# Optimization experiments

Hardware: AMD Instinct MI355X
Metric: run time of the kernel (lower is better)

Reference implementation:

```python
import jax, jax.numpy as jnp
import numpy as np

N_NODES = 50000
N_EDGES = 800000
F_IN, HID, N_CLASS = 128, 256, 40


def setup_inputs() -> dict:
    key = jax.random.key(0)
    ks = jax.random.split(key, 8)
    scale = lambda sh: 1.0 / np.sqrt(sh[-1]).astype(np.float32)
    x = jax.random.normal(ks[0], (N_NODES, F_IN), jnp.float32)
    edge_index = jax.random.randint(ks[1], (2, N_EDGES), 0, N_NODES, dtype=jnp.int64)
    W1l = jax.random.normal(ks[2], (HID, F_IN), jnp.float32) * scale((HID, F_IN))
    W1r = jax.random.normal(ks[3], (HID, F_IN), jnp.float32) * scale((HID, F_IN))
    b1 = jax.random.normal(ks[4], (HID,), jnp.float32) * 0.01
    W2l = jax.random.normal(ks[5], (N_CLASS, HID), jnp.float32) * scale((N_CLASS, HID))
    W2r = jax.random.normal(ks[6], (N_CLASS, HID), jnp.float32) * scale((N_CLASS, HID))
    b2 = jax.random.normal(ks[7], (N_CLASS,), jnp.float32) * 0.01
    return {"x": x, "edge_index": edge_index, "W1l": W1l, "b1": b1, "W1r": W1r,
            "W2l": W2l, "b2": b2, "W2r": W2r}


def sage_conv(x, edge_index, Wl, b, Wr):
    """PyG SAGEConv: lin_l(mean_{j->i} x_j) + lin_r(x_i); bias only on lin_l."""
    src, dst = edge_index[0], edge_index[1]
    # gather source node features -> segment mean at destination
    agg = jax.ops.segment_sum(x[src], dst, num_segments=N_NODES)
    deg = jax.ops.segment_sum(jnp.ones((edge_index.shape[1],), x.dtype), dst,
                              num_segments=N_NODES)
    mean = agg / jnp.maximum(deg, 1.0)[:, None]
    return mean @ Wl.T + b + x @ Wr.T


def reference(x, edge_index, W1l, b1, W1r, W2l, b2, W2r):
    h = jax.nn.relu(sage_conv(x, edge_index, W1l, b1, W1r))
    # dropout is identity in eval mode
    logits = sage_conv(h, edge_index, W2l, b2, W2r)
    return jax.nn.log_softmax(logits, axis=1)
```

## Files before the change

kernel.cpp:

```cpp
#include <hip/hip_runtime.h>
#include <hip/hip_bf16.h>
#include <float.h>

#define NN 50000
#define NE 800000
#define FIN 128
#define HID 256
#define NC 40
#define NBKT 196
#define BCAP 5120
#define EPB 4096

typedef __attribute__((ext_vector_type(8))) short bf16x8;
typedef __attribute__((ext_vector_type(4))) float f32x4;

__device__ __forceinline__ float bf2f(unsigned short u) {
  union { unsigned int i; float f; } v; v.i = ((unsigned int)u) << 16; return v.f;
}
__device__ __forceinline__ float lo_bf(unsigned int u) {
  union { unsigned int i; float f; } v; v.i = u << 16; return v.f;
}
__device__ __forceinline__ float hi_bf(unsigned int u) {
  union { unsigned int i; float f; } v; v.i = u & 0xffff0000u; return v.f;
}
__device__ __forceinline__ unsigned short f2bf(float f) {
  union { float f; unsigned int u; } v; v.f = f;
  unsigned int u = v.u;
  unsigned int r = u + 0x7fffu + ((u >> 16) & 1u);
  return (unsigned short)(r >> 16);
}

__global__ __launch_bounds__(256) void k_prep(const float* __restrict__ x,
                                              unsigned short* __restrict__ xb,
                                              const float* __restrict__ W1l,
                                              const float* __restrict__ W1r,
                                              unsigned short* __restrict__ w1t,
                                              const float* __restrict__ W2l,
                                              const float* __restrict__ W2r,
                                              unsigned short* __restrict__ w2t) {
  int tid = blockIdx.x * 256 + threadIdx.x;
  if (tid < NN * FIN / 4) {
    float4 v = ((const float4*)x)[tid];
    ushort4 o;
    o.x = f2bf(v.x); o.y = f2bf(v.y); o.z = f2bf(v.z); o.w = f2bf(v.w);
    ((ushort4*)xb)[tid] = o;
  }
  if (tid < HID * 256) {
    int j = tid >> 8, k = tid & 255;
    float v = (k < FIN) ? W1l[j * FIN + k] : W1r[j * FIN + (k - FIN)];
    w1t[tid] = f2bf(v);
  }
  if (tid < 80 * HID) {
    int j = tid >> 8, k = tid & 255;
    float v = (j < NC) ? W2l[j * HID + k] : W2r[(j - NC) * HID + k];
    w2t[tid] = f2bf(v);
  }
}

__global__ __launch_bounds__(512) void k_part(const int* __restrict__ src,
                                              const int* __restrict__ dst,
                                              int* __restrict__ bucket_cursor,
                                              unsigned int* __restrict__ pairs) {
  __shared__ int cnt[NBKT], cbase[NBKT], cur[NBKT];
  int t = threadIdx.x;
  for (int i = t; i < NBKT; i += 512) cnt[i] = 0;
  __syncthreads();
  int base = blockIdx.x * EPB;
  int myb[8];
  unsigned int mypk[8];
  #pragma unroll
  for (int k = 0; k < 8; ++k) {
    int e = base + k * 512 + t;
    myb[k] = -1;
    if (e < NE) {
      int d = dst[e];
      int b = d >> 8;
      myb[k] = b;
      mypk[k] = (unsigned int)src[e] | ((unsigned int)(d & 255) << 24);
      atomicAdd(&cnt[b], 1);
    }
  }
  __syncthreads();
  for (int i = t; i < NBKT; i += 512) {
    cur[i] = 0;
    cbase[i] = cnt[i] ? atomicAdd(&bucket_cursor[i], cnt[i]) : 0;
  }
  __syncthreads();
  #pragma unroll
  for (int k = 0; k < 8; ++k) {
    if (myb[k] >= 0) {
      int l = atomicAdd(&cur[myb[k]], 1);
      pairs[myb[k] * BCAP + cbase[myb[k]] + l] = mypk[k];
    }
  }
}

__global__ __launch_bounds__(256) void k_bscan(const int* __restrict__ bucket_cursor,
                                               int* __restrict__ bucket_base,
                                               int* __restrict__ rowptr) {
  __shared__ int sm[256];
  int t = threadIdx.x;
  int v = (t < NBKT) ? bucket_cursor[t] : 0;
  sm[t] = v;
  __syncthreads();
  for (int off = 1; off < 256; off <<= 1) {
    int u = (t >= off) ? sm[t - off] : 0;
    __syncthreads();
    sm[t] += u;
    __syncthreads();
  }
  bucket_base[t] = sm[t] - v;
  if (t == 0) rowptr[NN] = NE;
}

__global__ __launch_bounds__(512) void k_build(const int* __restrict__ bucket_base,
                                               const unsigned int* __restrict__ pairs,
                                               int* __restrict__ rowptr,
                                               float* __restrict__ rdeg,
                                               int* __restrict__ eidx) {
  __shared__ int hist[256], lbase[256], cur[256];
  int t = threadIdx.x;
  int b = blockIdx.x;
  int bb = bucket_base[b];
  int n  = bucket_base[b + 1] - bb;
  if (t < 256) hist[t] = 0;
  __syncthreads();
  unsigned int held[10];
  #pragma unroll
  for (int k = 0; k < 10; ++k) {
    int i = t + k * 512;
    unsigned int p = 0xFFFFFFFFu;
    if (i < n) {
      p = pairs[b * BCAP + i];
      atomicAdd(&hist[p >> 24], 1);
    }
    held[k] = p;
  }
  __syncthreads();
  int v = 0;
  if (t < 256) { v = hist[t]; lbase[t] = v; }
  __syncthreads();
  for (int off = 1; off < 256; off <<= 1) {
    int u = 0;
    if (t < 256 && t >= off) u = lbase[t - off];
    __syncthreads();
    if (t < 256) lbase[t] += u;
    __syncthreads();
  }
  if (t < 256) {
    int excl = lbase[t] - v;
    cur[t] = excl;
    int node = b * 256 + t;
    if (node < NN) {
      rowptr[node] = bb + excl;
      rdeg[node] = 1.0f / fmaxf((float)v, 1.0f);
    }
  }
  __syncthreads();
  #pragma unroll
  for (int k = 0; k < 10; ++k) {
    unsigned int p = held[k];
    if (p != 0xFFFFFFFFu) {
      int l = atomicAdd(&cur[p >> 24], 1);
      eidx[bb + l] = (int)(p & 0x00FFFFFFu);
    }
  }
}

__global__ __launch_bounds__(256) void k_agg1(const int* __restrict__ rowptr,
                                              const int* __restrict__ eidx,
                                              const float* __restrict__ rdeg,
                                              const unsigned int* __restrict__ xb,
                                              unsigned int* __restrict__ mean_bf) {
  int wid = threadIdx.x >> 6, lane = threadIdx.x & 63;
  int n = blockIdx.x * 4 + wid;
  if (n >= NN) return;
  int beg = rowptr[n], end = rowptr[n + 1];
  float ax = 0.f, ay = 0.f;
  int e = beg;
  for (; e + 8 <= end; e += 8) {
    int s0 = eidx[e],     s1 = eidx[e + 1], s2 = eidx[e + 2], s3 = eidx[e + 3];
    int s4 = eidx[e + 4], s5 = eidx[e + 5], s6 = eidx[e + 6], s7 = eidx[e + 7];
    unsigned int v0 = xb[s0 * 64 + lane], v1 = xb[s1 * 64 + lane];
    unsigned int v2 = xb[s2 * 64 + lane], v3 = xb[s3 * 64 + lane];
    unsigned int v4 = xb[s4 * 64 + lane], v5 = xb[s5 * 64 + lane];
    unsigned int v6 = xb[s6 * 64 + lane], v7 = xb[s7 * 64 + lane];
    ax += ((lo_bf(v0) + lo_bf(v1)) + (lo_bf(v2) + lo_bf(v3)))
        + ((lo_bf(v4) + lo_bf(v5)) + (lo_bf(v6) + lo_bf(v7)));
    ay += ((hi_bf(v0) + hi_bf(v1)) + (hi_bf(v2) + hi_bf(v3)))
        + ((hi_bf(v4) + hi_bf(v5)) + (hi_bf(v6) + hi_bf(v7)));
  }
  for (; e < end; ++e) {
    unsigned int v = xb[eidx[e] * 64 + lane];
    ax += lo_bf(v); ay += hi_bf(v);
  }
  float r = rdeg[n];
  unsigned int o = (unsigned int)f2bf(ax * r) | ((unsigned int)f2bf(ay * r) << 16);
  mean_bf[n * 64 + lane] = o;
}

__global__ __launch_bounds__(512, 4) void k_l12(const unsigned short* __restrict__ mean_bf,
                                                const unsigned short* __restrict__ x_bf,
                                                const unsigned short* __restrict__ w1t,
                                                const float* __restrict__ b1,
                                                const unsigned short* __restrict__ w2t,
                                                const float* __restrict__ b2,
                                                unsigned short* __restrict__ yl_bf,
                                                float* __restrict__ yr) {
  __shared__ unsigned short As[64][264];
  __shared__ unsigned short Ht[64][264];
  int t = threadIdx.x;
  int lane = t & 63, wave = t >> 6;
  int i0 = blockIdx.x * 64;
  #pragma unroll
  for (int u = 0; u < 4; ++u) {
    int idx = t + u * 512;
    int row = idx >> 5, q = idx & 31, k = q * 8;
    int gi = i0 + row;
    uint4 v = make_uint4(0, 0, 0, 0);
    if (gi < NN)
      v = *(const uint4*)((k < FIN) ? (mean_bf + gi * FIN + k)
                                    : (x_bf + gi * FIN + (k - FIN)));
    *(uint4*)&As[row][q * 8] = v;
  }
  __syncthreads();
  int fr = lane & 15, fq = lane >> 4, fk = fq * 8;
  f32x4 acc[4][2] = {};
  #pragma unroll
  for (int k0 = 0; k0 < HID; k0 += 32) {
    bf16x8 a[4], b[2];
    #pragma unroll
    for (int m = 0; m < 4; ++m) a[m] = *(const bf16x8*)&As[m * 16 + fr][k0 + fk];
    #pragma unroll
    for (int n = 0; n < 2; ++n)
      b[n] = *(const bf16x8*)(w1t + (wave * 32 + n * 16 + fr) * 256 + k0 + fk);
    #pragma unroll
    for (int m = 0; m < 4; ++m)
      #pragma unroll
      for (int n = 0; n < 2; ++n)
        acc[m][n] = __builtin_amdgcn_mfma_f32_16x16x32_bf16(a[m], b[n], acc[m][n], 0, 0, 0);
  }
  #pragma unroll
  for (int n = 0; n < 2; ++n) {
    int col = wave * 32 + n * 16 + fr;
    float bias = b1[col];
    #pragma unroll
    for (int m = 0; m < 4; ++m)
      #pragma unroll
      for (int r = 0; r < 4; ++r)
        Ht[m * 16 + fq * 4 + r][col] = f2bf(fmaxf(acc[m][n][r] + bias, 0.f));
  }
  __syncthreads();
  if (wave < 5) {
    f32x4 acc2[4] = {};
    #pragma unroll
    for (int k0 = 0; k0 < HID; k0 += 32) {
      bf16x8 b = *(const bf16x8*)(w2t + (wave * 16 + fr) * 256 + k0 + fk);
      #pragma unroll
      for (int m = 0; m < 4; ++m) {
        bf16x8 a = *(const bf16x8*)&Ht[m * 16 + fr][k0 + fk];
        acc2[m] = __builtin_amdgcn_mfma_f32_16x16x32_bf16(a, b, acc2[m], 0, 0, 0);
      }
    }
    int j = wave * 16 + fr;
    float badd = (j >= NC) ? b2[j - NC] : 0.f;
    #pragma unroll
    for (int m = 0; m < 4; ++m)
      #pragma unroll
      for (int r = 0; r < 4; ++r) {
        int i = i0 + m * 16 + fq * 4 + r;
        if (i < NN) {
          if (j < NC) yl_bf[i * NC + j] = f2bf(acc2[m][r]);
          else        yr[i * NC + (j - NC)] = acc2[m][r] + badd;
        }
      }
  }
}

__global__ __launch_bounds__(256) void k_final(const int* __restrict__ rowptr,
                                               const int* __restrict__ eidx,
                                               const float* __restrict__ rdeg,
                                               const unsigned short* __restrict__ yl_bf,
                                               const float* __restrict__ yr,
                                               float* __restrict__ out) {
  int wid  = threadIdx.x >> 6;
  int lane = threadIdx.x & 63;
  int row  = blockIdx.x * 4 + wid;
  if (row >= NN) return;
  int beg = rowptr[row], end = rowptr[row + 1];
  float logit = 0.f, v = -FLT_MAX;
  if (lane < NC) {
    float acc = 0.f;
    int e = beg;
    for (; e + 8 <= end; e += 8) {
      int s0 = eidx[e],     s1 = eidx[e + 1], s2 = eidx[e + 2], s3 = eidx[e + 3];
      int s4 = eidx[e + 4], s5 = eidx[e + 5], s6 = eidx[e + 6], s7 = eidx[e + 7];
      unsigned short a0 = yl_bf[s0 * NC + lane], a1 = yl_bf[s1 * NC + lane];
      unsigned short a2 = yl_bf[s2 * NC + lane], a3 = yl_bf[s3 * NC + lane];
      unsigned short a4 = yl_bf[s4 * NC + lane], a5 = yl_bf[s5 * NC + lane];
      unsigned short a6 = yl_bf[s6 * NC + lane], a7 = yl_bf[s7 * NC + lane];
      acc += ((bf2f(a0) + bf2f(a1)) + (bf2f(a2) + bf2f(a3)))
           + ((bf2f(a4) + bf2f(a5)) + (bf2f(a6) + bf2f(a7)));
    }
    for (; e < end; ++e) acc += bf2f(yl_bf[eidx[e] * NC + lane]);
    logit = acc * rdeg[row] + yr[row * NC + lane];
    v = logit;
  }
  #pragma unroll
  for (int o = 32; o > 0; o >>= 1) v = fmaxf(v, __shfl_xor(v, o, 64));
  float m = v;
  float s = (lane < NC) ? expf(logit - m) : 0.f;
  #pragma unroll
  for (int o = 32; o > 0; o >>= 1) s += __shfl_xor(s, o, 64);
  float lse = logf(s);
  if (lane < NC) out[row * NC + lane] = logit - m - lse;
}

extern "C" void kernel_launch(void* const* d_in, const int* in_sizes, int n_in,
                              void* d_out, int out_size, void* d_ws, size_t ws_size,
                              hipStream_t stream) {
  const float* x   = (const float*)d_in[0];
  const int*   ei  = (const int*)d_in[1];
  const float* W1l = (const float*)d_in[2];
  const float* b1  = (const float*)d_in[3];
  const float* W1r = (const float*)d_in[4];
  const float* W2l = (const float*)d_in[5];
  const float* b2  = (const float*)d_in[6];
  const float* W2r = (const float*)d_in[7];
  const int* src = ei;
  const int* dst = ei + NE;

  char* ws = (char*)d_ws;
  int*            rowptr  = (int*)(ws);
  float*          rdeg    = (float*)(ws + 200064);
  int*            bcursor = (int*)(ws + 400064);
  int*            bbase   = (int*)(ws + 401088);
  unsigned int*   pairs   = (unsigned int*)(ws + 402112);
  int*            eidx    = (int*)(ws + 4416192);
  unsigned short* x_bf    = (unsigned short*)(ws + 7616192);
  unsigned short* mean_bf = (unsigned short*)(ws + 20416192);
  unsigned short* w1t     = (unsigned short*)(ws + 33216192);
  unsigned short* yl_bf   = (unsigned short*)(ws + 33347264);
  float*          yr      = (float*)(ws + 37347264);
  unsigned short* w2t     = (unsigned short*)(ws + 45347264);

  hipMemsetAsync(bcursor, 0, 1024, stream);

  k_prep<<<(NN * FIN / 4 + 255) / 256, 256, 0, stream>>>(x, x_bf, W1l, W1r, w1t,
                                                         W2l, W2r, w2t);
  k_part<<<(NE + EPB - 1) / EPB, 512, 0, stream>>>(src, dst, bcursor, pairs);
  k_bscan<<<1, 256, 0, stream>>>(bcursor, bbase, rowptr);
  k_build<<<NBKT, 512, 0, stream>>>(bbase, pairs, rowptr, rdeg, eidx);
  k_agg1<<<(NN + 3) / 4, 256, 0, stream>>>(rowptr, eidx, rdeg, (const unsigned int*)x_bf,
                                           (unsigned int*)mean_bf);
  k_l12<<<(NN + 63) / 64, 512, 0, stream>>>(mean_bf, x_bf, w1t, b1, w2t, b2, yl_bf, yr);
  k_final<<<NN / 4, 256, 0, stream>>>(rowptr, eidx, rdeg, yl_bf, yr, (float*)d_out);
}
```

Baseline: 218.3 us.

## Fuse prep with partition, fold bucket scan into build, deepen gather unroll

```diff
diff --git a/kernel.cpp b/kernel.cpp
--- a/kernel.cpp
+++ b/kernel.cpp
@@ -9,7 +9,8 @@
 #define NC 40
 #define NBKT 196
 #define BCAP 5120
-#define EPB 4096
+#define EPB 1024
+#define NPART 782
 
 typedef __attribute__((ext_vector_type(8))) short bf16x8;
 typedef __attribute__((ext_vector_type(4))) float f32x4;
@@ -30,46 +31,45 @@
   return (unsigned short)(r >> 16);
 }
 
-__global__ __launch_bounds__(256) void k_prep(const float* __restrict__ x,
-                                              unsigned short* __restrict__ xb,
-                                              const float* __restrict__ W1l,
-                                              const float* __restrict__ W1r,
-                                              unsigned short* __restrict__ w1t,
-                                              const float* __restrict__ W2l,
-                                              const float* __restrict__ W2r,
-                                              unsigned short* __restrict__ w2t) {
-  int tid = blockIdx.x * 256 + threadIdx.x;
-  if (tid < NN * FIN / 4) {
-    float4 v = ((const float4*)x)[tid];
+__global__ __launch_bounds__(512) void k_partprep(const int* __restrict__ src,
+                                                  const int* __restrict__ dst,
+                                                  int* __restrict__ bucket_cursor,
+                                                  unsigned int* __restrict__ pairs,
+                                                  const float* __restrict__ x,
+                                                  unsigned short* __restrict__ xb,
+                                                  const float* __restrict__ W1l,
+                                                  const float* __restrict__ W1r,
+                                                  unsigned short* __restrict__ w1t,
+                                                  const float* __restrict__ W2l,
+                                                  const float* __restrict__ W2r,
+                                                  unsigned short* __restrict__ w2t) {
+  const int GT = NPART * 512;
+  int gt = blockIdx.x * 512 + threadIdx.x;
+  for (int i = gt; i < NN * FIN / 4; i += GT) {
+    float4 v = ((const float4*)x)[i];
     ushort4 o;
     o.x = f2bf(v.x); o.y = f2bf(v.y); o.z = f2bf(v.z); o.w = f2bf(v.w);
-    ((ushort4*)xb)[tid] = o;
-  }
-  if (tid < HID * 256) {
-    int j = tid >> 8, k = tid & 255;
+    ((ushort4*)xb)[i] = o;
+  }
+  if (gt < HID * 256) {
+    int j = gt >> 8, k = gt & 255;
     float v = (k < FIN) ? W1l[j * FIN + k] : W1r[j * FIN + (k - FIN)];
-    w1t[tid] = f2bf(v);
-  }
-  if (tid < 80 * HID) {
-    int j = tid >> 8, k = tid & 255;
+    w1t[gt] = f2bf(v);
+  }
+  if (gt < 80 * HID) {
+    int j = gt >> 8, k = gt & 255;
     float v = (j < NC) ? W2l[j * HID + k] : W2r[(j - NC) * HID + k];
-    w2t[tid] = f2bf(v);
-  }
-}
-
-__global__ __launch_bounds__(512) void k_part(const int* __restrict__ src,
-                                              const int* __restrict__ dst,
-                                              int* __restrict__ bucket_cursor,
-                                              unsigned int* __restrict__ pairs) {
+    w2t[gt] = f2bf(v);
+  }
   __shared__ int cnt[NBKT], cbase[NBKT], cur[NBKT];
   int t = threadIdx.x;
   for (int i = t; i < NBKT; i += 512) cnt[i] = 0;
   __syncthreads();
   int base = blockIdx.x * EPB;
-  int myb[8];
-  unsigned int mypk[8];
-  #pragma unroll
-  for (int k = 0; k < 8; ++k) {
+  int myb[2];
+  unsigned int mypk[2];
+  #pragma unroll
+  for (int k = 0; k < 2; ++k) {
     int e = base + k * 512 + t;
     myb[k] = -1;
     if (e < NE) {
@@ -87,7 +87,7 @@
   }
   __syncthreads();
   #pragma unroll
-  for (int k = 0; k < 8; ++k) {
+  for (int k = 0; k < 2; ++k) {
     if (myb[k] >= 0) {
       int l = atomicAdd(&cur[myb[k]], 1);
       pairs[myb[k] * BCAP + cbase[myb[k]] + l] = mypk[k];
@@ -95,34 +95,30 @@
   }
 }
 
-__global__ __launch_bounds__(256) void k_bscan(const int* __restrict__ bucket_cursor,
-                                               int* __restrict__ bucket_base,
-                                               int* __restrict__ rowptr) {
-  __shared__ int sm[256];
-  int t = threadIdx.x;
-  int v = (t < NBKT) ? bucket_cursor[t] : 0;
-  sm[t] = v;
-  __syncthreads();
-  for (int off = 1; off < 256; off <<= 1) {
-    int u = (t >= off) ? sm[t - off] : 0;
-    __syncthreads();
-    sm[t] += u;
-    __syncthreads();
-  }
-  bucket_base[t] = sm[t] - v;
-  if (t == 0) rowptr[NN] = NE;
-}
-
-__global__ __launch_bounds__(512) void k_build(const int* __restrict__ bucket_base,
+__global__ __launch_bounds__(512) void k_build(const int* __restrict__ bucket_cursor,
                                                const unsigned int* __restrict__ pairs,
                                                int* __restrict__ rowptr,
                                                float* __restrict__ rdeg,
                                                int* __restrict__ eidx) {
+  __shared__ int sm[256];
   __shared__ int hist[256], lbase[256], cur[256];
   int t = threadIdx.x;
   int b = blockIdx.x;
-  int bb = bucket_base[b];
-  int n  = bucket_base[b + 1] - bb;
+  int c = 0;
+  if (t < 256) {
+    c = (t < NBKT) ? bucket_cursor[t] : 0;
+    sm[t] = c;
+  }
+  __syncthreads();
+  for (int off = 1; off < 256; off <<= 1) {
+    int u = 0;
+    if (t < 256 && t >= off) u = sm[t - off];
+    __syncthreads();
+    if (t < 256) sm[t] += u;
+    __syncthreads();
+  }
+  int bb = (b > 0) ? sm[b - 1] : 0;
+  int n  = sm[b] - bb;
   if (t < 256) hist[t] = 0;
   __syncthreads();
   unsigned int held[10];
@@ -156,6 +152,7 @@
       rdeg[node] = 1.0f / fmaxf((float)v, 1.0f);
     }
   }
+  if (b == NBKT - 1 && t == 0) rowptr[NN] = NE;
   __syncthreads();
   #pragma unroll
   for (int k = 0; k < 10; ++k) {
@@ -178,17 +175,29 @@
   int beg = rowptr[n], end = rowptr[n + 1];
   float ax = 0.f, ay = 0.f;
   int e = beg;
-  for (; e + 8 <= end; e += 8) {
-    int s0 = eidx[e],     s1 = eidx[e + 1], s2 = eidx[e + 2], s3 = eidx[e + 3];
-    int s4 = eidx[e + 4], s5 = eidx[e + 5], s6 = eidx[e + 6], s7 = eidx[e + 7];
-    unsigned int v0 = xb[s0 * 64 + lane], v1 = xb[s1 * 64 + lane];
-    unsigned int v2 = xb[s2 * 64 + lane], v3 = xb[s3 * 64 + lane];
-    unsigned int v4 = xb[s4 * 64 + lane], v5 = xb[s5 * 64 + lane];
-    unsigned int v6 = xb[s6 * 64 + lane], v7 = xb[s7 * 64 + lane];
-    ax += ((lo_bf(v0) + lo_bf(v1)) + (lo_bf(v2) + lo_bf(v3)))
-        + ((lo_bf(v4) + lo_bf(v5)) + (lo_bf(v6) + lo_bf(v7)));
-    ay += ((hi_bf(v0) + hi_bf(v1)) + (hi_bf(v2) + hi_bf(v3)))
-        + ((hi_bf(v4) + hi_bf(v5)) + (hi_bf(v6) + hi_bf(v7)));
+  for (; e + 16 <= end; e += 16) {
+    int s[16]; unsigned int v[16];
+    #pragma unroll
+    for (int k = 0; k < 16; ++k) s[k] = eidx[e + k];
+    #pragma unroll
+    for (int k = 0; k < 16; ++k) v[k] = xb[s[k] * 64 + lane];
+    float x0 = 0.f, x1 = 0.f, y0 = 0.f, y1 = 0.f;
+    #pragma unroll
+    for (int k = 0; k < 16; k += 2) {
+      x0 += lo_bf(v[k]);     y0 += hi_bf(v[k]);
+      x1 += lo_bf(v[k + 1]); y1 += hi_bf(v[k + 1]);
+    }
+    ax += x0 + x1; ay += y0 + y1;
+  }
+  if (e + 8 <= end) {
+    int s[8]; unsigned int v[8];
+    #pragma unroll
+    for (int k = 0; k < 8; ++k) s[k] = eidx[e + k];
+    #pragma unroll
+    for (int k = 0; k < 8; ++k) v[k] = xb[s[k] * 64 + lane];
+    #pragma unroll
+    for (int k = 0; k < 8; ++k) { ax += lo_bf(v[k]); ay += hi_bf(v[k]); }
+    e += 8;
   }
   for (; e < end; ++e) {
     unsigned int v = xb[eidx[e] * 64 + lane];
@@ -292,15 +301,26 @@
   if (lane < NC) {
     float acc = 0.f;
     int e = beg;
-    for (; e + 8 <= end; e += 8) {
-      int s0 = eidx[e],     s1 = eidx[e + 1], s2 = eidx[e + 2], s3 = eidx[e + 3];
-      int s4 = eidx[e + 4], s5 = eidx[e + 5], s6 = eidx[e + 6], s7 = eidx[e + 7];
-      unsigned short a0 = yl_bf[s0 * NC + lane], a1 = yl_bf[s1 * NC + lane];
-      unsigned short a2 = yl_bf[s2 * NC + lane], a3 = yl_bf[s3 * NC + lane];
-      unsigned short a4 = yl_bf[s4 * NC + lane], a5 = yl_bf[s5 * NC + lane];
-      unsigned short a6 = yl_bf[s6 * NC + lane], a7 = yl_bf[s7 * NC + lane];
-      acc += ((bf2f(a0) + bf2f(a1)) + (bf2f(a2) + bf2f(a3)))
-           + ((bf2f(a4) + bf2f(a5)) + (bf2f(a6) + bf2f(a7)));
+    for (; e + 16 <= end; e += 16) {
+      int s[16]; unsigned short a[16];
+      #pragma unroll
+      for (int k = 0; k < 16; ++k) s[k] = eidx[e + k];
+      #pragma unroll
+      for (int k = 0; k < 16; ++k) a[k] = yl_bf[s[k] * NC + lane];
+      float a0 = 0.f, a1 = 0.f;
+      #pragma unroll
+      for (int k = 0; k < 16; k += 2) { a0 += bf2f(a[k]); a1 += bf2f(a[k + 1]); }
+      acc += a0 + a1;
+    }
+    if (e + 8 <= end) {
+      int s[8]; unsigned short a[8];
+      #pragma unroll
+      for (int k = 0; k < 8; ++k) s[k] = eidx[e + k];
+      #pragma unroll
+      for (int k = 0; k < 8; ++k) a[k] = yl_bf[s[k] * NC + lane];
+      #pragma unroll
+      for (int k = 0; k < 8; ++k) acc += bf2f(a[k]);
+      e += 8;
     }
     for (; e < end; ++e) acc += bf2f(yl_bf[eidx[e] * NC + lane]);
     logit = acc * rdeg[row] + yr[row * NC + lane];
@@ -334,7 +354,6 @@
   int*            rowptr  = (int*)(ws);
   float*          rdeg    = (float*)(ws + 200064);
   int*            bcursor = (int*)(ws + 400064);
-  int*            bbase   = (int*)(ws + 401088);
   unsigned int*   pairs   = (unsigned int*)(ws + 402112);
   int*            eidx    = (int*)(ws + 4416192);
   unsigned short* x_bf    = (unsigned short*)(ws + 7616192);
@@ -346,11 +365,9 @@
 
   hipMemsetAsync(bcursor, 0, 1024, stream);
 
-  k_prep<<<(NN * FIN / 4 + 255) / 256, 256, 0, stream>>>(x, x_bf, W1l, W1r, w1t,
-                                                         W2l, W2r, w2t);
-  k_part<<<(NE + EPB - 1) / EPB, 512, 0, stream>>>(src, dst, bcursor, pairs);
-  k_bscan<<<1, 256, 0, stream>>>(bcursor, bbase, rowptr);
-  k_build<<<NBKT, 512, 0, stream>>>(bbase, pairs, rowptr, rdeg, eidx);
+  k_partprep<<<NPART, 512, 0, stream>>>(src, dst, bcursor, pairs,
+                                        x, x_bf, W1l, W1r, w1t, W2l, W2r, w2t);
+  k_build<<<NBKT, 512, 0, stream>>>(bcursor, pairs, rowptr, rdeg, eidx);
   k_agg1<<<(NN + 3) / 4, 256, 0, stream>>>(rowptr, eidx, rdeg, (const unsigned int*)x_bf,
                                            (unsigned int*)mean_bf);
   k_l12<<<(NN + 63) / 64, 512, 0, stream>>>(mean_bf, x_bf, w1t, b1, w2t, b2, yl_bf, yr);
```

After: 218.1 us. Within noise of the previous version (-0.1%).
